# Performance work log

Hardware: AMD Instinct MI355X
Metric: run time of the kernel (lower is better)

Reference implementation:

```python
import jax, jax.numpy as jnp
import numpy as np

INF = 1.0e9
MU = 1e-8
SAFE_THRESHOLD = 0.05
B = 128
N = 512            # NORMALIZED_SIZE
OBS = 8            # observation steps
PARTITIONS = 8
MAX_PARTITIONS = 16
VISION_RADIUS = 2.0
TWO_PI = 2.0 * np.pi


def setup_inputs() -> dict:
    key = jax.random.key(0)
    k1, k2, k3, k4, k5 = jax.random.split(key, 5)
    # segmentation maps in [0, 1]; values <= 0.05 are 'safe' pixels
    seg_maps = jax.random.uniform(k1, (B, N, N), dtype=jnp.float32)
    # paras: W (pixels-per-meter scale) in [2.5, 3.5], b (pixel offset) in [0, 20]
    Wscale = jax.random.uniform(k2, (B, 2), dtype=jnp.float32, minval=2.5, maxval=3.5)
    boffs = jax.random.uniform(k3, (B, 2), dtype=jnp.float32, minval=0.0, maxval=20.0)
    seg_map_paras = jnp.concatenate([Wscale, boffs], axis=-1)  # [B, 4]
    trajectories = 2.0 * jax.random.normal(k4, (B, OBS, 2), dtype=jnp.float32)
    # reference points near the middle of the (meters-space) map
    current_pos = 80.0 + 5.0 * jax.random.normal(k5, (B, 1, 2), dtype=jnp.float32)
    # pixel-center grid (pool_size = 1 -> map_pos_pixel = pixel indices)
    xs, ys = jnp.meshgrid(jnp.arange(N), jnp.arange(N), indexing='ij')
    map_pos_pixel = jnp.stack([xs.reshape(-1), ys.reshape(-1)], axis=-1).astype(jnp.float32)  # [N*N, 2]
    return {
        'seg_maps': seg_maps,
        'seg_map_paras': seg_map_paras,
        'trajectories': trajectories,
        'current_pos': current_pos,
        'map_pos_pixel': map_pos_pixel,
    }


def reference(seg_maps, seg_map_paras, trajectories, current_pos, map_pos_pixel):
    b = seg_maps.shape[0]
    _obs = trajectories + current_pos                        # [B, OBS, 2]
    maps_flat = seg_maps.reshape(b, -1)                      # [B, P]
    safe = maps_flat <= SAFE_THRESHOLD                       # [B, P] bool

    moving_vector = _obs[:, -1, :] - _obs[:, 0, :]           # [B, 2]
    moving_length = jnp.linalg.norm(moving_vector, axis=-1)  # [B]

    Wp = seg_map_paras[:, None, :2]                          # [B, 1, 2]
    bp = seg_map_paras[:, None, 2:4]                         # [B, 1, 2]
    map_pos = (map_pos_pixel[None] - bp) / Wp                # [B, P, 2]

    dvec = map_pos - current_pos                             # [B, P, 2]
    dist = jnp.linalg.norm(dvec, axis=-1)                    # [B, P]
    angles = jnp.arctan2(dvec[..., 0], dvec[..., 1])         # [B, P]
    bin_idx = ((angles % TWO_PI) / (TWO_PI / PARTITIONS)).astype(jnp.int32)  # [B, P]

    equ_dis = (dist + MU) / (maps_flat + MU)                 # [B, P]
    r = (VISION_RADIUS * moving_length)[:, None]             # [B, 1]
    valid = (~safe) & (dist <= r)                            # [B, P]
    d = jnp.where(valid, equ_dis, INF)                       # [B, P]

    # single-pass per-angle-bin min (replaces the per-partition Python loop)
    seg_min = jax.vmap(
        lambda dv, bi: jax.ops.segment_min(dv, bi, num_segments=PARTITIONS)
    )(d, bin_idx)                                            # [B, K]
    min_d = jnp.minimum(seg_min, INF)                        # empty segments -> INF
    obstacle = (min_d < INF).astype(d.dtype)                 # [B, K]

    f_velocity = moving_length[:, None] * obstacle           # [B, K]
    f_min_distance = min_d * obstacle                        # [B, K]
    centers = (TWO_PI * (jnp.arange(PARTITIONS, dtype=d.dtype) + 0.5) / PARTITIONS)
    f_direction = centers[None, :] * obstacle                # [B, K]

    pc = jnp.stack([f_velocity, f_min_distance, f_direction], axis=-1)  # [B, K, 3]
    pc = jnp.pad(pc, ((0, 0), (0, MAX_PARTITIONS - PARTITIONS), (0, 0)))
    return pc
```

## Files before the change

### kernel.cpp

```cpp
#include <hip/hip_runtime.h>
#include <math.h>

#define BATCH 128
#define NN 512
#define PARTS 8
#define INF_F 1000000000.0f
#define MU_F 1e-8f
#define SAFE_T 0.05f
#define TWO_PI_F 6.28318530717958647692f
#define STEP_F 0.78539816339744830962f

__global__ __launch_bounds__(256) void pc_kernel(
    const float* __restrict__ seg_maps,
    const float* __restrict__ paras,
    const float* __restrict__ traj,
    const float* __restrict__ cpos,
    float* __restrict__ out)
{
    const int b   = blockIdx.x;
    const int tid = threadIdx.x;

    const float Wx = paras[b * 4 + 0];
    const float Wy = paras[b * 4 + 1];
    const float bx = paras[b * 4 + 2];
    const float by = paras[b * 4 + 3];
    const float cx = cpos[b * 2 + 0];
    const float cy = cpos[b * 2 + 1];

    const float o0x = traj[b * 16 + 0]  + cx;
    const float o0y = traj[b * 16 + 1]  + cy;
    const float o7x = traj[b * 16 + 14] + cx;
    const float o7y = traj[b * 16 + 15] + cy;
    const float mvx = o7x - o0x;
    const float mvy = o7y - o0y;
    const float ml  = __fsqrt_rn(__fadd_rn(__fmul_rn(mvx, mvx), __fmul_rn(mvy, mvy)));
    const float r   = 2.0f * ml;

    int ilo = (int)floorf(bx + Wx * (cx - r)) - 2;
    int ihi = (int)ceilf (bx + Wx * (cx + r)) + 2;
    int jlo = (int)floorf(by + Wy * (cy - r)) - 2;
    int jhi = (int)ceilf (by + Wy * (cy + r)) + 2;
    ilo = max(ilo, 0); ihi = min(ihi, NN - 1);
    jlo = max(jlo, 0); jhi = min(jhi, NN - 1);

    float mind[PARTS];
#pragma unroll
    for (int k = 0; k < PARTS; ++k) mind[k] = INF_F;

    if (ilo <= ihi && jlo <= jhi) {
        const int w     = jhi - jlo + 1;
        const int h     = ihi - ilo + 1;
        const int count = w * h;
        const float* mb = seg_maps + (size_t)b * NN * NN;

        for (int t = tid; t < count; t += 256) {
            const int i = ilo + t / w;
            const int j = jlo + t % w;

            const float dx = __fdiv_rn((float)i - bx, Wx) - cx;
            const float dy = __fdiv_rn((float)j - by, Wy) - cy;
            const float s  = __fadd_rn(__fmul_rn(dx, dx), __fmul_rn(dy, dy));
            const float dist = __fsqrt_rn(s);

            const float m = mb[i * NN + j];
            if (m > SAFE_T && dist <= r) {
                const float ang = atan2f(dx, dy);
                const float am  = (ang < 0.0f) ? (ang + (float)TWO_PI_F) : ang;
                const int bin   = (int)__fdiv_rn(am, (float)STEP_F);
                if (bin < PARTS) {
                    const float ed = __fdiv_rn(dist + MU_F, m + MU_F);
                    mind[bin] = fminf(mind[bin], ed);
                }
            }
        }
    }

    __shared__ float red[4 * PARTS];
    const int lane = tid & 63;
    const int wave = tid >> 6;
#pragma unroll
    for (int k = 0; k < PARTS; ++k) {
        float v = mind[k];
#pragma unroll
        for (int off = 32; off >= 1; off >>= 1)
            v = fminf(v, __shfl_xor(v, off, 64));
        if (lane == 0) red[wave * PARTS + k] = v;
    }
    __syncthreads();

    if (tid < 48) {
        const int k = tid / 3;
        const int c = tid % 3;
        float val = 0.0f;
        if (k < PARTS) {
            const float mn = fminf(fminf(red[0 * PARTS + k], red[1 * PARTS + k]),
                                   fminf(red[2 * PARTS + k], red[3 * PARTS + k]));
            if (mn < INF_F) {
                if (c == 0)      val = ml;
                else if (c == 1) val = mn;
                else             val = __fdiv_rn(__fmul_rn((float)TWO_PI_F, (float)k + 0.5f), 8.0f);
            }
        }
        out[b * 48 + k * 3 + c] = val;
    }
}

extern "C" void kernel_launch(void* const* d_in, const int* in_sizes, int n_in,
                              void* d_out, int out_size, void* d_ws, size_t ws_size,
                              hipStream_t stream) {
    const float* seg_maps = (const float*)d_in[0];
    const float* paras    = (const float*)d_in[1];
    const float* traj     = (const float*)d_in[2];
    const float* cpos     = (const float*)d_in[3];

    pc_kernel<<<BATCH, 256, 0, stream>>>(seg_maps, paras, traj, cpos, (float*)d_out);
}
```

Baseline: 196.7 us.

## Precompute per-row/column map coordinates in shared memory and widen blocks to 1024 threads

Each block now has 1024 threads instead of 256. The per-axis map coordinates (dx for rows, dy for columns) are computed once into shared memory instead of recomputing two correctly rounded divisions per pixel. The flat index loop with integer div/mod becomes a 2D loop: wave-lane maps to columns for coalescing and the wave index strides rows. The aim is to cut per-pixel ALU work and raise per-block memory parallelism, since only 128 blocks run. In exchange it adds a shared-memory pass, a barrier, and a 16-wave reduction, and the larger block size may raise register pressure.

```diff
diff --git a/kernel.cpp b/kernel.cpp
--- a/kernel.cpp
+++ b/kernel.cpp
@@ -9,8 +9,9 @@
 #define SAFE_T 0.05f
 #define TWO_PI_F 6.28318530717958647692f
 #define STEP_F 0.78539816339744830962f
+#define NT 1024
 
-__global__ __launch_bounds__(256) void pc_kernel(
+__global__ __launch_bounds__(NT) void pc_kernel(
     const float* __restrict__ seg_maps,
     const float* __restrict__ paras,
     const float* __restrict__ traj,
@@ -43,39 +44,51 @@
     ilo = max(ilo, 0); ihi = min(ihi, NN - 1);
     jlo = max(jlo, 0); jhi = min(jhi, NN - 1);
 
+    int h = 0, w = 0;
+    if (ilo <= ihi && jlo <= jhi) {
+        h = ihi - ilo + 1;
+        w = jhi - jlo + 1;
+    }
+
+    __shared__ float dxs[NN];
+    __shared__ float dys[NN];
+    for (int t = tid; t < h; t += NT)
+        dxs[t] = __fdiv_rn((float)(ilo + t) - bx, Wx) - cx;
+    for (int t = tid; t < w; t += NT)
+        dys[t] = __fdiv_rn((float)(jlo + t) - by, Wy) - cy;
+    __syncthreads();
+
     float mind[PARTS];
 #pragma unroll
     for (int k = 0; k < PARTS; ++k) mind[k] = INF_F;
 
-    if (ilo <= ihi && jlo <= jhi) {
-        const int w     = jhi - jlo + 1;
-        const int h     = ihi - ilo + 1;
-        const int count = w * h;
+    if (h > 0) {
         const float* mb = seg_maps + (size_t)b * NN * NN;
+        const int ti = tid >> 6;
+        const int tj = tid & 63;
 
-        for (int t = tid; t < count; t += 256) {
-            const int i = ilo + t / w;
-            const int j = jlo + t % w;
-
-            const float dx = __fdiv_rn((float)i - bx, Wx) - cx;
-            const float dy = __fdiv_rn((float)j - by, Wy) - cy;
-            const float s  = __fadd_rn(__fmul_rn(dx, dx), __fmul_rn(dy, dy));
-            const float dist = __fsqrt_rn(s);
-
-            const float m = mb[i * NN + j];
-            if (m > SAFE_T && dist <= r) {
-                const float ang = atan2f(dx, dy);
-                const float am  = (ang < 0.0f) ? (ang + (float)TWO_PI_F) : ang;
-                const int bin   = (int)__fdiv_rn(am, (float)STEP_F);
-                if (bin < PARTS) {
-                    const float ed = __fdiv_rn(dist + MU_F, m + MU_F);
-                    mind[bin] = fminf(mind[bin], ed);
+        for (int jj = tj; jj < w; jj += 64) {
+            const float dy = dys[jj];
+            const int j = jlo + jj;
+            for (int ii = ti; ii < h; ii += 16) {
+                const float dx = dxs[ii];
+                const float m  = mb[(ilo + ii) * NN + j];
+                const float s  = __fadd_rn(__fmul_rn(dx, dx), __fmul_rn(dy, dy));
+                const float dist = __fsqrt_rn(s);
+                if (m > SAFE_T && dist <= r) {
+                    const float ang = atan2f(dx, dy);
+                    const float am  = (ang < 0.0f) ? (ang + (float)TWO_PI_F) : ang;
+                    const int bin   = (int)__fdiv_rn(am, (float)STEP_F);
+                    if (bin < PARTS) {
+                        const float ed = __fdiv_rn(dist + MU_F, m + MU_F);
+                        mind[bin] = fminf(mind[bin], ed);
+                    }
                 }
             }
         }
     }
 
-    __shared__ float red[4 * PARTS];
+    __shared__ float red[16 * PARTS];
     const int lane = tid & 63;
     const int wave = tid >> 6;
 #pragma unroll
@@ -93,8 +106,10 @@
         const int c = tid % 3;
         float val = 0.0f;
         if (k < PARTS) {
-            const float mn = fminf(fminf(red[0 * PARTS + k], red[1 * PARTS + k]),
-                                   fminf(red[2 * PARTS + k], red[3 * PARTS + k]));
+            float mn = INF_F;
+#pragma unroll
+            for (int wv = 0; wv < 16; ++wv)
+                mn = fminf(mn, red[wv * PARTS + k]);
             if (mn < INF_F) {
                 if (c == 0)      val = ml;
                 else if (c == 1) val = mn;
@@ -113,5 +128,5 @@
     const float* traj     = (const float*)d_in[2];
     const float* cpos     = (const float*)d_in[3];
 
-    pc_kernel<<<BATCH, 256, 0, stream>>>(seg_maps, paras, traj, cpos, (float*)d_out);
+    pc_kernel<<<BATCH, NT, 0, stream>>>(seg_maps, paras, traj, cpos, (float*)d_out);
 }
```

Result: faster. 177.2 us (-9.9%).
